# Kernel tuning notes

Hardware: AMD Instinct MI355X
Metric: run time of the kernel (lower is better)

## Reference

```python
import jax, jax.numpy as jnp
import numpy as np

B, T, H, O, L = 64, 512, 256, 128, 2


def setup_inputs() -> dict:
    key = jax.random.key(0)
    ks = jax.random.split(key, 12)
    s = lambda k, shape, scale=0.05: jax.random.normal(k, shape, dtype=jnp.float32) * scale
    return {
        "encoder_outputs": jax.random.normal(ks[0], (B, T, H), dtype=jnp.float32),
        "h0": jax.random.normal(ks[1], (L, B, H), dtype=jnp.float32),
        "c0": jax.random.normal(ks[2], (L, B, H), dtype=jnp.float32),
        "actions": jax.random.randint(ks[3], (B, T), 0, O, dtype=jnp.int32),
        "embedding": jax.random.uniform(ks[4], (O, H), dtype=jnp.float32, minval=-1.0, maxval=1.0),
        "Wih": s(ks[5], (L, 4 * H, H)),
        "Whh": s(ks[6], (L, 4 * H, H)),
        "bih": jnp.zeros((L, 4 * H), jnp.float32),
        "bhh": jnp.zeros((L, 4 * H), jnp.float32),
        "W_attn": s(ks[7], (H, H)),
        "b_attn": jnp.zeros((H,), jnp.float32),
        "W_concat": s(ks[8], (H, 2 * H)),
        "b_concat": jnp.zeros((H,), jnp.float32),
        "W_out": s(ks[9], (O, H)),
        "W_critic": s(ks[10], (O, O)),
        "b_critic": jnp.zeros((O,), jnp.float32),
    }


def _run_lstm(x, h0, c0, Wih, Whh, bih, bhh):
    # x: [B, T, H]; stacked-layer LSTM, PyTorch gate order (i, f, g, o)
    xs = jnp.swapaxes(x, 0, 1)  # [T, B, H]
    for l in range(Wih.shape[0]):
        Wi_l, Wh_l = Wih[l].T, Whh[l].T
        b_l = bih[l] + bhh[l]
        def step(carry, xt, Wi=Wi_l, Wh=Wh_l, b=b_l):
            h, c = carry
            g = xt @ Wi + h @ Wh + b
            i, f, gg, o = jnp.split(g, 4, axis=-1)
            c = jax.nn.sigmoid(f) * c + jax.nn.sigmoid(i) * jnp.tanh(gg)
            h = jax.nn.sigmoid(o) * jnp.tanh(c)
            return (h, c), h
        _, xs = jax.lax.scan(step, (h0[l], c0[l]), xs)
    return jnp.swapaxes(xs, 0, 1)  # [B, T, H]


def reference(encoder_outputs, h0, c0, actions, embedding, Wih, Whh, bih, bhh,
              W_attn, b_attn, W_concat, b_concat, W_out, W_critic, b_critic):
    # Teacher forcing: input at step t is action[t-1], step 0 input is token 0.
    ids = jnp.concatenate([jnp.zeros((actions.shape[0], 1), actions.dtype), actions[:, :-1]], axis=1)
    emb = embedding[ids]  # [B, T, H]
    out = _run_lstm(emb, h0, c0, Wih, Whh, bih, bhh)  # [B, T, H]

    # Luong attention, batched over all decode steps (same math as per-step bmm)
    keys = encoder_outputs @ W_attn.T + b_attn  # [B, S, H]
    scores = jnp.einsum("bth,bsh->bts", out, keys)
    weights = jax.nn.softmax(scores, axis=-1)
    ctx = jnp.einsum("bts,bsh->bth", weights, encoder_outputs)
    out = jnp.tanh(jnp.concatenate([out, ctx], axis=-1) @ W_concat.T + b_concat)

    logits = out @ W_out.T  # [B, T, O]
    qvalues = logits @ W_critic.T + b_critic  # [B, T, O]
    values = jnp.sum(qvalues * logits, axis=-1)  # [B, T]
    decoder_action = actions.astype(jnp.float32)
    return decoder_action, logits, values
```

## Files before the change

kernel.cpp:

```cpp
#include <hip/hip_runtime.h>
#include <stdint.h>

#define BB   64
#define TT   512
#define HT   256
#define OO   128
#define GATES 1024

#define PREG 10
#define PLDS 4
#define PSTR 2
#define UREG (2*PREG)
#define ULDS (2*PLDS)
#define AGDEPTH 16

typedef _Float16 half_t;
typedef _Float16 half2_t __attribute__((ext_vector_type(2)));
typedef float    f32x4  __attribute__((ext_vector_type(4)));
typedef unsigned long long u64;

__device__ __forceinline__ half2_t h2_(unsigned int x) {
    return __builtin_bit_cast(half2_t, x);
}
#define WG_BARRIER() do { __builtin_amdgcn_s_waitcnt(0xC07F); \
                          __builtin_amdgcn_s_barrier(); } while (0)

__device__ __forceinline__ float fast_sig(float x) {
    return __builtin_amdgcn_rcpf(1.0f + __expf(-x));
}
__device__ __forceinline__ float fast_tanh(float x) {
    float t = __expf(2.0f * x);
    return 1.0f - 2.0f * __builtin_amdgcn_rcpf(t + 1.0f);
}

__device__ __forceinline__ unsigned int scload(const unsigned int* p) {
    unsigned long long a = (unsigned long long)p;
    unsigned int w;
    asm volatile("global_load_dword %0, %1, off sc0 sc1\n\ts_waitcnt vmcnt(0)"
                 : "=v"(w) : "v"(a) : "memory");
    return w;
}
__device__ __forceinline__ u64 scload64(const u64* p) {
    unsigned long long a = (unsigned long long)p;
    u64 w;
    asm volatile("global_load_dwordx2 %0, %1, off sc0 sc1\n\ts_waitcnt vmcnt(0)"
                 : "=v"(w) : "v"(a) : "memory");
    return w;
}
__device__ __forceinline__ void scload64x4(
    const u64* p0, const u64* p1, const u64* p2, const u64* p3,
    u64& w0, u64& w1, u64& w2, u64& w3)
{
    unsigned long long a0 = (unsigned long long)p0;
    unsigned long long a1 = (unsigned long long)p1;
    unsigned long long a2 = (unsigned long long)p2;
    unsigned long long a3 = (unsigned long long)p3;
    asm volatile(
        "global_load_dwordx2 %0, %4, off sc0 sc1\n\t"
        "global_load_dwordx2 %1, %5, off sc0 sc1\n\t"
        "global_load_dwordx2 %2, %6, off sc0 sc1\n\t"
        "global_load_dwordx2 %3, %7, off sc0 sc1\n\t"
        "s_waitcnt vmcnt(0)"
        : "=v"(w0), "=v"(w1), "=v"(w2), "=v"(w3)
        : "v"(a0), "v"(a1), "v"(a2), "v"(a3) : "memory");
}

#define PAIR_DOT(wa0, wb0, wa1, wb1, h4)                                  \
    do {                                                                   \
        a0 = __builtin_amdgcn_fdot2(h2_((wa0).x), h2_((h4).x), a0, false); \
        a0 = __builtin_amdgcn_fdot2(h2_((wa0).y), h2_((h4).y), a0, false); \
        a1 = __builtin_amdgcn_fdot2(h2_((wa0).z), h2_((h4).x), a1, false); \
        a1 = __builtin_amdgcn_fdot2(h2_((wa0).w), h2_((h4).y), a1, false); \
        a2 = __builtin_amdgcn_fdot2(h2_((wb0).x), h2_((h4).x), a2, false); \
        a2 = __builtin_amdgcn_fdot2(h2_((wb0).y), h2_((h4).y), a2, false); \
        a3 = __builtin_amdgcn_fdot2(h2_((wb0).z), h2_((h4).x), a3, false); \
        a3 = __builtin_amdgcn_fdot2(h2_((wb0).w), h2_((h4).y), a3, false); \
        a0 = __builtin_amdgcn_fdot2(h2_((wa1).x), h2_((h4).z), a0, false); \
        a0 = __builtin_amdgcn_fdot2(h2_((wa1).y), h2_((h4).w), a0, false); \
        a1 = __builtin_amdgcn_fdot2(h2_((wa1).z), h2_((h4).z), a1, false); \
        a1 = __builtin_amdgcn_fdot2(h2_((wa1).w), h2_((h4).w), a1, false); \
        a2 = __builtin_amdgcn_fdot2(h2_((wb1).x), h2_((h4).z), a2, false); \
        a2 = __builtin_amdgcn_fdot2(h2_((wb1).y), h2_((h4).w), a2, false); \
        a3 = __builtin_amdgcn_fdot2(h2_((wb1).z), h2_((h4).z), a3, false); \
        a3 = __builtin_amdgcn_fdot2(h2_((wb1).w), h2_((h4).w), a3, false); \
    } while (0)

#define DOT_PHASE()                                                        \
    do {                                                                   \
        _Pragma("unroll 2")                                                \
        for (int p = 0; p < PSTR; p++) {                                   \
            uint4 wa0 = Ws[(p * 4 + 0) * 512 + tid];                       \
            uint4 wb0 = Ws[(p * 4 + 1) * 512 + tid];                       \
            uint4 wa1 = Ws[(p * 4 + 2) * 512 + tid];                       \
            uint4 wb1 = Ws[(p * 4 + 3) * 512 + tid];                       \
            uint4 h4  = hp4[hb + PREG + PLDS + p];                         \
            PAIR_DOT(wa0, wb0, wa1, wb1, h4);                              \
        }                                                                  \
        _Pragma("unroll")                                                  \
        for (int p = 0; p < PLDS; p++) {                                   \
            uint4 wa0 = Wlh[(p * 4 + 0) * 512 + tid];                      \
            uint4 wb0 = Wlh[(p * 4 + 1) * 512 + tid];                      \
            uint4 wa1 = Wlh[(p * 4 + 2) * 512 + tid];                      \
            uint4 wb1 = Wlh[(p * 4 + 3) * 512 + tid];                      \
            uint4 h4  = hp4[hb + PREG + p];                                \
            PAIR_DOT(wa0, wb0, wa1, wb1, h4);                              \
        }                                                                  \
        _Pragma("unroll")                                                  \
        for (int p = 0; p < PREG; p++) {                                   \
            uint4 h4 = hp4[hb + p];                                        \
            PAIR_DOT(wreg[4 * p], wreg[4 * p + 1],                         \
                     wreg[4 * p + 2], wreg[4 * p + 3], h4);                \
        }                                                                  \
    } while (0)

__global__ __launch_bounds__(256) void embed_kernel(
    const int* __restrict__ actions, const float* __restrict__ emb_table,
    float* __restrict__ X, float* __restrict__ dact)
{
    int row = blockIdx.x;
    int t = row & (TT - 1);
    int id = (t == 0) ? 0 : actions[row - 1];
    X[(int64_t)row * HT + threadIdx.x] = emb_table[(int64_t)id * HT + threadIdx.x];
    if (threadIdx.x == 0) dact[row] = (float)actions[row];
}

__global__ __launch_bounds__(256) void repack_w_kernel(
    const float* __restrict__ Whh, const float* __restrict__ Wih,
    uint4* __restrict__ Wpkh)
{
    int idx = blockIdx.x * 256 + threadIdx.x;
    int g   = idx & 32767;
    int l   = idx >> 15;
    int tid = g & 511;
    int ab  = (g >> 9) & 1;
    int u   = (g >> 10) & 31;
    int s = tid >> 8, q = tid & 255;
    int r0 = 4 * q + 2 * ab;
    int k  = 128 * s + 4 * u;
    const float* base = (l == 0) ? Whh
                      : (l == 1) ? Whh + (int64_t)GATES * HT
                                 : Wih + (int64_t)GATES * HT;
    const float4 a = *(const float4*)(base + (int64_t)r0 * HT + k);
    const float4 b = *(const float4*)(base + (int64_t)(r0 + 1) * HT + k);
    half2_t p0 = {(half_t)a.x, (half_t)a.y};
    half2_t p1 = {(half_t)a.z, (half_t)a.w};
    half2_t p2 = {(half_t)b.x, (half_t)b.y};
    half2_t p3 = {(half_t)b.z, (half_t)b.w};
    uint4 o;
    o.x = __builtin_bit_cast(unsigned int, p0);
    o.y = __builtin_bit_cast(unsigned int, p1);
    o.z = __builtin_bit_cast(unsigned int, p2);
    o.w = __builtin_bit_cast(unsigned int, p3);
    Wpkh[idx] = o;
}

__global__ __launch_bounds__(256) void hxzero_kernel(
    uint4* __restrict__ HX4, u64* __restrict__ AGU,
    unsigned int* __restrict__ CCTR)
{
    int i = blockIdx.x * 256 + threadIdx.x;
    HX4[i] = make_uint4(0u, 0u, 0u, 0u);
    if (i < AGDEPTH * 64 * 1024) AGU[i] = 0ull;
    if (i < 64) CCTR[i] = 0u;
}

template<bool TRANS_B, int ACT>
__global__ __launch_bounds__(256) void mfma_gemm_kernel(
    const float* __restrict__ A, const float* __restrict__ Bm,
    float* __restrict__ C,
    int K, int lda, int ldb, int ldc,
    int64_t sA, int64_t sB, int64_t sC,
    const float* __restrict__ bias1, const float* __restrict__ bias2)
{
    constexpr int BM = 128, BN = 128, BK = 32;
    constexpr int LDT = BK + 8;
    __shared__ __align__(16) half_t Asl[BM * LDT];
    __shared__ __align__(16) half_t Bsl[BN * LDT];

    const int tid  = threadIdx.x;
    const int wave = tid >> 6;
    const int lane = tid & 63;
    const int wm = (wave & 1) * 64;
    const int wn = (wave >> 1) * 64;
    const int m0 = blockIdx.y * BM;
    const int n0 = blockIdx.x * BN;
    A  += (int64_t)blockIdx.z * sA;
    Bm += (int64_t)blockIdx.z * sB;
    C  += (int64_t)blockIdx.z * sC;

    const int fm = lane & 15;
    const int qd = lane >> 4;

    f32x4 acc[4][4] = {};

    for (int k0 = 0; k0 < K; k0 += BK) {
        #pragma unroll
        for (int i = 0; i < 4; i++) {
            int idx = tid + i * 256;
            int r  = idx >> 3;
            int kq = idx & 7;
            float4 v = *(const float4*)(A + (int64_t)(m0 + r) * lda + k0 + kq * 4);
            half_t* d = &Asl[r * LDT + kq * 4];
            d[0] = (half_t)v.x; d[1] = (half_t)v.y;
            d[2] = (half_t)v.z; d[3] = (half_t)v.w;
        }
        if (TRANS_B) {
            #pragma unroll
            for (int i = 0; i < 4; i++) {
                int idx = tid + i * 256;
                int r  = idx >> 3;
                int kq = idx & 7;
                float4 v = *(const float4*)(Bm + (int64_t)(n0 + r) * ldb + k0 + kq * 4);
                half_t* d = &Bsl[r * LDT + kq * 4];
                d[0] = (half_t)v.x; d[1] = (half_t)v.y;
                d[2] = (half_t)v.z; d[3] = (half_t)v.w;
            }
        } else {
            #pragma unroll
            for (int i = 0; i < 4; i++) {
                int idx = tid + i * 256;
                int kk = idx >> 5;
                int nq = idx & 31;
                float4 v = *(const float4*)(Bm + (int64_t)(k0 + kk) * ldb + n0 + nq * 4);
                Bsl[(nq * 4 + 0) * LDT + kk] = (half_t)v.x;
                Bsl[(nq * 4 + 1) * LDT + kk] = (half_t)v.y;
                Bsl[(nq * 4 + 2) * LDT + kk] = (half_t)v.z;
                Bsl[(nq * 4 + 3) * LDT + kk] = (half_t)v.w;
            }
        }
        __syncthreads();

        typedef _Float16 f16x8 __attribute__((ext_vector_type(8)));
        f16x8 af[4], bf[4];
        #pragma unroll
        for (int t = 0; t < 4; t++)
            af[t] = *(const f16x8*)&Asl[(wm + t * 16 + fm) * LDT + qd * 8];
        #pragma unroll
        for (int t = 0; t < 4; t++)
            bf[t] = *(const f16x8*)&Bsl[(wn + t * 16 + fm) * LDT + qd * 8];
        #pragma unroll
        for (int mt = 0; mt < 4; mt++)
            #pragma unroll
            for (int nt = 0; nt < 4; nt++)
                acc[mt][nt] = __builtin_amdgcn_mfma_f32_16x16x32_f16(
                                  af[mt], bf[nt], acc[mt][nt], 0, 0, 0);
        __syncthreads();
    }

    #pragma unroll
    for (int nt = 0; nt < 4; nt++) {
        int n = n0 + wn + nt * 16 + fm;
        float bv = 0.0f;
        if (bias1) bv += bias1[n];
        if (bias2) bv += bias2[n];
        #pragma unroll
        for (int mt = 0; mt < 4; mt++) {
            #pragma unroll
            for (int r = 0; r < 4; r++) {
                int m = m0 + wm + mt * 16 + qd * 4 + r;
                float v = acc[mt][nt][r] + bv;
                if (ACT == 1) v = tanhf(v);
                C[(int64_t)m * ldc + n] = v;
            }
        }
    }
}

template<bool TRANS_B, int ACT>
__global__ __launch_bounds__(256) void gemm128_kernel(
    const float* __restrict__ A, const float* __restrict__ Bm,
    float* __restrict__ C,
    int K, int lda, int ldb, int ldc,
    int64_t sA, int64_t sB, int64_t sC,
    const float* __restrict__ bias1, const float* __restrict__ bias2)
{
    constexpr int BM = 128, BN = 128, BK = 16;
    __shared__ __align__(16) float As[BK][BM + 4];
    __shared__ __align__(16) float Bs[BK][BN + 4];

    const int tid = threadIdx.x;
    const int m0 = blockIdx.y * BM;
    const int n0 = blockIdx.x * BN;
    A  += (int64_t)blockIdx.z * sA;
    Bm += (int64_t)blockIdx.z * sB;
    C  += (int64_t)blockIdx.z * sC;

    const int tm = tid & 15;
    const int tn = tid >> 4;

    float acc[8][8] = {};

    for (int k0 = 0; k0 < K; k0 += BK) {
        #pragma unroll
        for (int i = 0; i < 2; i++) {
            int idx = tid + i * 256;
            int ar = idx >> 2;
            int ak = (idx & 3) * 4;
            const float4 v = *(const float4*)(A + (int64_t)(m0 + ar) * lda + k0 + ak);
            As[ak + 0][ar] = v.x; As[ak + 1][ar] = v.y;
            As[ak + 2][ar] = v.z; As[ak + 3][ar] = v.w;
        }
        if (TRANS_B) {
            #pragma unroll
            for (int i = 0; i < 2; i++) {
                int idx = tid + i * 256;
                int br = idx >> 2;
                int bk = (idx & 3) * 4;
                const float4 v = *(const float4*)(Bm + (int64_t)(n0 + br) * ldb + k0 + bk);
                Bs[bk + 0][br] = v.x; Bs[bk + 1][br] = v.y;
                Bs[bk + 2][br] = v.z; Bs[bk + 3][br] = v.w;
            }
        } else {
            #pragma unroll
            for (int i = 0; i < 2; i++) {
                int idx = tid + i * 256;
                int bk = idx >> 5;
                int bn = (idx & 31) * 4;
                const float4 v = *(const float4*)(Bm + (int64_t)(k0 + bk) * ldb + n0 + bn);
                *(float4*)&Bs[bk][bn] = v;
            }
        }
        __syncthreads();

        #pragma unroll
        for (int k = 0; k < BK; k++) {
            float a[8], b[8];
            *(float4*)&a[0] = *(const float4*)&As[k][tm * 8];
            *(float4*)&a[4] = *(const float4*)&As[k][tm * 8 + 4];
            *(float4*)&b[0] = *(const float4*)&Bs[k][tn * 8];
            *(float4*)&b[4] = *(const float4*)&Bs[k][tn * 8 + 4];
            #pragma unroll
            for (int i = 0; i < 8; i++)
                #pragma unroll
                for (int j = 0; j < 8; j++)
                    acc[i][j] += a[i] * b[j];
        }
        __syncthreads();
    }

    float bv[8];
    #pragma unroll
    for (int j = 0; j < 8; j++) {
        int n = n0 + tn * 8 + j;
        float b = 0.0f;
        if (bias1) b += bias1[n];
        if (bias2) b += bias2[n];
        bv[j] = b;
    }
    #pragma unroll
    for (int i = 0; i < 8; i++) {
        int64_t m = m0 + tm * 8 + i;
        float o[8];
        #pragma unroll
        for (int j = 0; j < 8; j++) {
            float v = acc[i][j] + bv[j];
            if (ACT == 1) v = tanhf(v);
            o[j] = v;
        }
        *(float4*)(C + m * ldc + n0 + tn * 8)     = make_float4(o[0], o[1], o[2], o[3]);
        *(float4*)(C + m * ldc + n0 + tn * 8 + 4) = make_float4(o[4], o[5], o[6], o[7]);
    }
}

__global__ __launch_bounds__(512)
__attribute__((amdgpu_waves_per_eu(2, 2)))
void fused_rec_kernel(
    const float* __restrict__ Ag0,
    const uint4* __restrict__ Wpk,
    const float* __restrict__ h0l,
    const float* __restrict__ c0l,
    const float* __restrict__ bih,
    const float* __restrict__ bhh,
    float* __restrict__ cat,
    unsigned int* __restrict__ HX,
    u64* __restrict__ AGU,
    unsigned int* __restrict__ CCTR)
{
    const int bid  = blockIdx.x;
    const int role = bid >> 6;
    const int b    = bid & 63;
    const int tid  = threadIdx.x;
    const int s    = tid >> 8;
    const int q    = tid & 255;

    __shared__ __align__(16) uint4          Wlh[ULDS * 2 * 512];
    __shared__ __align__(16) float          gsh2[2 * GATES];
    __shared__ __align__(16) float          agsh[2][GATES];
    __shared__ __align__(16) unsigned short hsh[HT];

    const uint4* Wb = Wpk + (role == 0 ? 0 : (role == 1 ? 2 : 1)) * 32768;

    uint4 wreg[2 * UREG];
    #pragma unroll
    for (int u = 0; u < UREG; u++) {
        wreg[2 * u]     = Wb[(u * 2 + 0) * 512 + tid];
        wreg[2 * u + 1] = Wb[(u * 2 + 1) * 512 + tid];
    }
    #pragma unroll
    for (int v = 0; v < ULDS; v++) {
        Wlh[(v * 2 + 0) * 512 + tid] = Wb[((UREG + v) * 2 + 0) * 512 + tid];
        Wlh[(v * 2 + 1) * 512 + tid] = Wb[((UREG + v) * 2 + 1) * 512 + tid];
    }
    const uint4* __restrict__ Ws = Wb + (UREG + ULDS) * 2 * 512;
    const uint4* hp4 = (const uint4*)hsh;
    const int hb = 16 * s;

    if (role == 0) {
        if (tid < HT) {
            half_t hv = (half_t)h0l[b * HT + tid];
            hsh[tid] = __builtin_bit_cast(unsigned short, hv);
        }
        float c = (tid < HT) ? c0l[b * HT + tid] : 0.0f;
        const float* AgB = Ag0 + (int64_t)b * TT * GATES;
        unsigned int* HXb = HX + (int64_t)b * TT * HT;
        __syncthreads();

        #pragma unroll 1
        for (int st = 0; st < TT; st++) {
            float4 aval = make_float4(0.f, 0.f, 0.f, 0.f);
            if (s == 0) aval = *(const float4*)(AgB + (int64_t)st * GATES + 4 * q);
            float a0 = 0.f, a1 = 0.f, a2 = 0.f, a3 = 0.f;
            DOT_PHASE();
            a0 += aval.x; a1 += aval.y; a2 += aval.z; a3 += aval.w;
            *(float4*)&gsh2[s * GATES + 4 * q] = make_float4(a0, a1, a2, a3);
            WG_BARRIER();
            if (tid < HT) {
                float gi = gsh2[tid]          + gsh2[GATES + tid];
                float gf = gsh2[HT + tid]     + gsh2[GATES + HT + tid];
                float gg = gsh2[2 * HT + tid] + gsh2[GATES + 2 * HT + tid];
                float go = gsh2[3 * HT + tid] + gsh2[GATES + 3 * HT + tid];
                c = fast_sig(gf) * c + fast_sig(gi) * fast_tanh(gg);
                float h = fast_sig(go) * fast_tanh(c);
                half_t hh = (half_t)h;
                unsigned short hb16 = __builtin_bit_cast(unsigned short, hh);
                hsh[tid] = hb16;
                atomicExch(HXb + (int64_t)st * HT + tid,
                           ((unsigned)(st + 1) << 16) | (unsigned)hb16);
            }
            WG_BARRIER();
        }
    } else if (role == 1) {
        float bi_ = 0.f, bf_ = 0.f, bg_ = 0.f, bo_ = 0.f;
        if (tid < HT) {
            bi_ = bih[GATES + tid]          + bhh[GATES + tid];
            bf_ = bih[GATES + HT + tid]     + bhh[GATES + HT + tid];
            bg_ = bih[GATES + 2 * HT + tid] + bhh[GATES + 2 * HT + tid];
            bo_ = bih[GATES + 3 * HT + tid] + bhh[GATES + 3 * HT + tid];
        }
        const unsigned int* HXb = HX + (int64_t)b * TT * HT;
        __syncthreads();

        #pragma unroll 1
        for (int st = 0; st < TT; st++) {
            if ((st & 3) == 0 && st >= AGDEPTH && tid == 0) {
                while (scload(&CCTR[b]) < (unsigned)(st - (AGDEPTH - 4))) {}
            }
            if (tid < HT) {
                const unsigned int* src = HXb + (int64_t)st * HT + tid;
                unsigned int w = scload(src);
                while ((w >> 16) != (unsigned)(st + 1)) w = scload(src);
                hsh[tid] = (unsigned short)(w & 0xffffu);
            }
            WG_BARRIER();
            float a0 = 0.f, a1 = 0.f, a2 = 0.f, a3 = 0.f;
            DOT_PHASE();
            *(float4*)&gsh2[s * GATES + 4 * q] = make_float4(a0, a1, a2, a3);
            WG_BARRIER();
            if (tid < HT) {
                u64 hi = ((u64)(st + 1)) << 32;
                u64* dst = AGU + (int64_t)((st & (AGDEPTH - 1)) * 64 + b) * 1024;
                float v0 = gsh2[tid]          + gsh2[GATES + tid]          + bi_;
                float v1 = gsh2[HT + tid]     + gsh2[GATES + HT + tid]     + bf_;
                float v2 = gsh2[2 * HT + tid] + gsh2[GATES + 2 * HT + tid] + bg_;
                float v3 = gsh2[3 * HT + tid] + gsh2[GATES + 3 * HT + tid] + bo_;
                atomicExch(&dst[tid],          hi | (u64)__float_as_uint(v0));
                atomicExch(&dst[HT + tid],     hi | (u64)__float_as_uint(v1));
                atomicExch(&dst[2 * HT + tid], hi | (u64)__float_as_uint(v2));
                atomicExch(&dst[3 * HT + tid], hi | (u64)__float_as_uint(v3));
            }
        }
    } else {
        if (tid < HT) {
            half_t hv = (half_t)h0l[BB * HT + b * HT + tid];
            hsh[tid] = __builtin_bit_cast(unsigned short, hv);
        }
        float c = (tid < HT) ? c0l[BB * HT + b * HT + tid] : 0.0f;
        __syncthreads();
        if (tid >= 256) {
            int i = tid - 256;
            const u64* src = AGU + (int64_t)b * 1024;
            u64 w0, w1, w2, w3;
            scload64x4(src + i, src + i + 256, src + i + 512, src + i + 768,
                       w0, w1, w2, w3);
            while ((unsigned)(w0 >> 32) != 1u) w0 = scload64(src + i);
            while ((unsigned)(w1 >> 32) != 1u) w1 = scload64(src + i + 256);
            while ((unsigned)(w2 >> 32) != 1u) w2 = scload64(src + i + 512);
            while ((unsigned)(w3 >> 32) != 1u) w3 = scload64(src + i + 768);
            agsh[0][i]       = __uint_as_float((unsigned)w0);
            agsh[0][i + 256] = __uint_as_float((unsigned)w1);
            agsh[0][i + 512] = __uint_as_float((unsigned)w2);
            agsh[0][i + 768] = __uint_as_float((unsigned)w3);
        }
        WG_BARRIER();

        #pragma unroll 1
        for (int st = 0; st < TT; st++) {
            float a0 = 0.f, a1 = 0.f, a2 = 0.f, a3 = 0.f;
            DOT_PHASE();
            *(float4*)&gsh2[s * GATES + 4 * q] = make_float4(a0, a1, a2, a3);
            WG_BARRIER();
            if (tid < HT) {
                const float* ag = agsh[st & 1];
                float gi = gsh2[tid]          + gsh2[GATES + tid]          + ag[tid];
                float gf = gsh2[HT + tid]     + gsh2[GATES + HT + tid]     + ag[HT + tid];
                float gg = gsh2[2 * HT + tid] + gsh2[GATES + 2 * HT + tid] + ag[2 * HT + tid];
                float go = gsh2[3 * HT + tid] + gsh2[GATES + 3 * HT + tid] + ag[3 * HT + tid];
                c = fast_sig(gf) * c + fast_sig(gi) * fast_tanh(gg);
                float h = fast_sig(go) * fast_tanh(c);
                hsh[tid] = __builtin_bit_cast(unsigned short, (half_t)h);
                cat[((int64_t)b * TT + st) * (2 * HT) + tid] = h;
            } else {
                if ((st & 3) == 3 && tid == 256)
                    atomicExch(&CCTR[b], (unsigned)(st + 1));
                if (st + 1 < TT) {
                    int i = tid - 256;
                    int sl = (st + 1) & (AGDEPTH - 1);
                    unsigned expect = (unsigned)(st + 2);
                    const u64* src = AGU + (int64_t)(sl * 64 + b) * 1024;
                    u64 w0, w1, w2, w3;
                    scload64x4(src + i, src + i + 256, src + i + 512, src + i + 768,
                               w0, w1, w2, w3);
                    while ((unsigned)(w0 >> 32) != expect) w0 = scload64(src + i);
                    while ((unsigned)(w1 >> 32) != expect) w1 = scload64(src + i + 256);
                    while ((unsigned)(w2 >> 32) != expect) w2 = scload64(src + i + 512);
                    while ((unsigned)(w3 >> 32) != expect) w3 = scload64(src + i + 768);
                    float* d = agsh[(st + 1) & 1];
                    d[i]       = __uint_as_float((unsigned)w0);
                    d[i + 256] = __uint_as_float((unsigned)w1);
                    d[i + 512] = __uint_as_float((unsigned)w2);
                    d[i + 768] = __uint_as_float((unsigned)w3);
                }
            }
            WG_BARRIER();
        }
    }
}

__global__ __launch_bounds__(256) void softmax512_kernel(float* __restrict__ S)
{
    int row = blockIdx.x * 4 + (threadIdx.x >> 6);
    int lane = threadIdx.x & 63;
    float* p = S + (int64_t)row * 512 + lane * 8;
    float4 v0 = *(float4*)p;
    float4 v1 = *(float4*)(p + 4);
    float m = fmaxf(fmaxf(fmaxf(v0.x, v0.y), fmaxf(v0.z, v0.w)),
                    fmaxf(fmaxf(v1.x, v1.y), fmaxf(v1.z, v1.w)));
    #pragma unroll
    for (int off = 32; off; off >>= 1) m = fmaxf(m, __shfl_xor(m, off));
    v0.x = __expf(v0.x - m); v0.y = __expf(v0.y - m);
    v0.z = __expf(v0.z - m); v0.w = __expf(v0.w - m);
    v1.x = __expf(v1.x - m); v1.y = __expf(v1.y - m);
    v1.z = __expf(v1.z - m); v1.w = __expf(v1.w - m);
    float s = v0.x + v0.y + v0.z + v0.w + v1.x + v1.y + v1.z + v1.w;
    #pragma unroll
    for (int off = 32; off; off >>= 1) s += __shfl_xor(s, off);
    float inv = 1.0f / s;
    v0.x *= inv; v0.y *= inv; v0.z *= inv; v0.w *= inv;
    v1.x *= inv; v1.y *= inv; v1.z *= inv; v1.w *= inv;
    *(float4*)p = v0;
    *(float4*)(p + 4) = v1;
}

__global__ __launch_bounds__(256) void values_kernel(
    const float* __restrict__ Q, const float* __restrict__ L, float* __restrict__ V)
{
    int row = blockIdx.x * 4 + (threadIdx.x >> 6);
    int lane = threadIdx.x & 63;
    float2 q = *(const float2*)(Q + (int64_t)row * OO + lane * 2);
    float2 l = *(const float2*)(L + (int64_t)row * OO + lane * 2);
    float s = q.x * l.x + q.y * l.y;
    #pragma unroll
    for (int off = 32; off; off >>= 1) s += __shfl_xor(s, off);
    if (lane == 0) V[row] = s;
}

extern "C" void kernel_launch(void* const* d_in, const int* in_sizes, int n_in,
                              void* d_out, int out_size, void* d_ws, size_t ws_size,
                              hipStream_t stream)
{
    const float* enc      = (const float*)d_in[0];
    const float* h0       = (const float*)d_in[1];
    const float* c0       = (const float*)d_in[2];
    const int*   actions  = (const int*)  d_in[3];
    const float* emb_t    = (const float*)d_in[4];
    const float* Wih      = (const float*)d_in[5];
    const float* Whh      = (const float*)d_in[6];
    const float* bih      = (const float*)d_in[7];
    const float* bhh      = (const float*)d_in[8];
    const float* W_attn   = (const float*)d_in[9];
    const float* b_attn   = (const float*)d_in[10];
    const float* W_concat = (const float*)d_in[11];
    const float* b_concat = (const float*)d_in[12];
    const float* W_out    = (const float*)d_in[13];
    const float* W_critic = (const float*)d_in[14];
    const float* b_critic = (const float*)d_in[15];
    (void)in_sizes; (void)n_in; (void)out_size; (void)ws_size;

    const int M = BB * TT;

    float* out    = (float*)d_out;
    float* dact   = out;
    float* logits = out + M;
    float* values = out + M + (int64_t)M * OO;

    float* ws    = (float*)d_ws;
    float* gates = ws;
    float* xbuf  = ws + 33554432;
    float* cat   = ws + 41943040;
    float* keysR = ws + 58720256;
    float* keys  = keysR;
    uint4* Wpkh  = (uint4*)keysR;
    u64*   AGU   = (u64*)(ws + 59500000);
    unsigned int* CCTR = (unsigned int*)(ws + 61600000);
    unsigned int* HX   = (unsigned int*)xbuf;
    float* scores = gates;
    float* qv     = gates;
    float* dec    = xbuf;

    hipLaunchKernelGGL(embed_kernel, dim3(M), dim3(256), 0, stream,
                       actions, emb_t, xbuf, dact);
    hipLaunchKernelGGL(repack_w_kernel, dim3(384), dim3(256), 0, stream,
                       Whh, Wih, Wpkh);
    hipLaunchKernelGGL((mfma_gemm_kernel<true, 0>), dim3(8, 256, 1), dim3(256), 0, stream,
                       xbuf, Wih, gates, HT, HT, HT, GATES,
                       (int64_t)0, (int64_t)0, (int64_t)0, bih, bhh);
    hipLaunchKernelGGL(hxzero_kernel, dim3(8192), dim3(256), 0, stream,
                       (uint4*)HX, AGU, CCTR);
    hipLaunchKernelGGL(fused_rec_kernel, dim3(192), dim3(512), 0, stream,
                       gates, Wpkh, h0, c0, bih, bhh, cat, HX, AGU, CCTR);
    hipLaunchKernelGGL((mfma_gemm_kernel<true, 0>), dim3(2, 256, 1), dim3(256), 0, stream,
                       enc, W_attn, keys, HT, HT, HT, HT,
                       (int64_t)0, (int64_t)0, (int64_t)0, b_attn, (const float*)nullptr);
    hipLaunchKernelGGL((mfma_gemm_kernel<true, 0>), dim3(4, 4, BB), dim3(256), 0, stream,
                       cat, keys, scores, HT, 2 * HT, HT, TT,
                       (int64_t)TT * 2 * HT, (int64_t)TT * HT, (int64_t)TT * TT,
                       (const float*)nullptr, (const float*)nullptr);
    hipLaunchKernelGGL(softmax512_kernel, dim3(M / 4), dim3(256), 0, stream, scores);
    hipLaunchKernelGGL((mfma_gemm_kernel<false, 0>), dim3(2, 4, BB), dim3(256), 0, stream,
                       scores, enc, cat + HT, TT, TT, HT, 2 * HT,
                       (int64_t)TT * TT, (int64_t)TT * HT, (int64_t)TT * 2 * HT,
                       (const float*)nullptr, (const float*)nullptr);
    hipLaunchKernelGGL((mfma_gemm_kernel<true, 1>), dim3(2, 256, 1), dim3(256), 0, stream,
                       cat, W_concat, dec, 2 * HT, 2 * HT, 2 * HT, HT,
                       (int64_t)0, (int64_t)0, (int64_t)0, b_concat, (const float*)nullptr);
    hipLaunchKernelGGL((gemm128_kernel<true, 0>), dim3(1, 256, 1), dim3(256), 0, stream,
                       dec, W_out, logits, HT, HT, HT, OO,
                       (int64_t)0, (int64_t)0, (int64_t)0,
                       (const float*)nullptr, (const float*)nullptr);
    hipLaunchKernelGGL((gemm128_kernel<true, 0>), dim3(1, 256, 1), dim3(256), 0, stream,
                       logits, W_critic, qv, OO, OO, OO, OO,
                       (int64_t)0, (int64_t)0, (int64_t)0, b_critic, (const float*)nullptr);
    hipLaunchKernelGGL(values_kernel, dim3(M / 4), dim3(256), 0, stream,
                       qv, logits, values);
}
```

Before: 1.615 ms.

## Split layer-1 input projection role across two blocks per batch and prefetch gates

The role that computes the layer-1 input projection (Wih[1] times layer-0 h) is now split across two workgroups per batch row, each handling 512 gate rows with a new weight packing. This halves per-block work on that stage of the wavefront pipeline, and the grid grows from 192 to 256 blocks. The layer-1 recurrence block also issues its polling loads for the next step's precomputed gates before its dot phase and waits on them afterwards, hiding global latency behind compute. The cost is more blocks that must stay co-resident for the spin-wait protocol, plus more atomic traffic.

```diff
diff --git a/kernel.cpp b/kernel.cpp
--- a/kernel.cpp
+++ b/kernel.cpp
@@ -63,6 +63,30 @@
         "s_waitcnt vmcnt(0)"
         : "=v"(w0), "=v"(w1), "=v"(w2), "=v"(w3)
         : "v"(a0), "v"(a1), "v"(a2), "v"(a3) : "memory");
+}
+__device__ __forceinline__ void scload64x4_issue(
+    const u64* p0, const u64* p1, const u64* p2, const u64* p3,
+    u64& w0, u64& w1, u64& w2, u64& w3)
+{
+    unsigned long long a0 = (unsigned long long)p0;
+    unsigned long long a1 = (unsigned long long)p1;
+    unsigned long long a2 = (unsigned long long)p2;
+    unsigned long long a3 = (unsigned long long)p3;
+    asm volatile(
+        "global_load_dwordx2 %0, %4, off sc0 sc1\n\t"
+        "global_load_dwordx2 %1, %5, off sc0 sc1\n\t"
+        "global_load_dwordx2 %2, %6, off sc0 sc1\n\t"
+        "global_load_dwordx2 %3, %7, off sc0 sc1"
+        : "=v"(w0), "=v"(w1), "=v"(w2), "=v"(w3)
+        : "v"(a0), "v"(a1), "v"(a2), "v"(a3) : "memory");
+}
+
+__device__ __forceinline__ float dot8(float acc, uint4 wv, uint4 h4) {
+    acc = __builtin_amdgcn_fdot2(h2_(wv.x), h2_(h4.x), acc, false);
+    acc = __builtin_amdgcn_fdot2(h2_(wv.y), h2_(h4.y), acc, false);
+    acc = __builtin_amdgcn_fdot2(h2_(wv.z), h2_(h4.z), acc, false);
+    acc = __builtin_amdgcn_fdot2(h2_(wv.w), h2_(h4.w), acc, false);
+    return acc;
 }
 
 #define PAIR_DOT(wa0, wb0, wa1, wb1, h4)                                  \
@@ -131,27 +155,51 @@
     int idx = blockIdx.x * 256 + threadIdx.x;
     int g   = idx & 32767;
     int l   = idx >> 15;
-    int tid = g & 511;
-    int ab  = (g >> 9) & 1;
-    int u   = (g >> 10) & 31;
-    int s = tid >> 8, q = tid & 255;
-    int r0 = 4 * q + 2 * ab;
-    int k  = 128 * s + 4 * u;
-    const float* base = (l == 0) ? Whh
-                      : (l == 1) ? Whh + (int64_t)GATES * HT
-                                 : Wih + (int64_t)GATES * HT;
-    const float4 a = *(const float4*)(base + (int64_t)r0 * HT + k);
-    const float4 b = *(const float4*)(base + (int64_t)(r0 + 1) * HT + k);
-    half2_t p0 = {(half_t)a.x, (half_t)a.y};
-    half2_t p1 = {(half_t)a.z, (half_t)a.w};
-    half2_t p2 = {(half_t)b.x, (half_t)b.y};
-    half2_t p3 = {(half_t)b.z, (half_t)b.w};
-    uint4 o;
-    o.x = __builtin_bit_cast(unsigned int, p0);
-    o.y = __builtin_bit_cast(unsigned int, p1);
-    o.z = __builtin_bit_cast(unsigned int, p2);
-    o.w = __builtin_bit_cast(unsigned int, p3);
-    Wpkh[idx] = o;
+    const float* base;
+    int row, k;
+    if (l < 2) {
+        int tid = g & 511;
+        int ab  = (g >> 9) & 1;
+        int u   = (g >> 10) & 31;
+        int s = tid >> 8, q = tid & 255;
+        row = 4 * q + 2 * ab;
+        k   = 128 * s + 4 * u;
+        base = Whh + (int64_t)l * (GATES * HT);
+        const float4 a = *(const float4*)(base + (int64_t)row * HT + k);
+        const float4 b = *(const float4*)(base + (int64_t)(row + 1) * HT + k);
+        half2_t p0 = {(half_t)a.x, (half_t)a.y};
+        half2_t p1 = {(half_t)a.z, (half_t)a.w};
+        half2_t p2 = {(half_t)b.x, (half_t)b.y};
+        half2_t p3 = {(half_t)b.z, (half_t)b.w};
+        uint4 o;
+        o.x = __builtin_bit_cast(unsigned int, p0);
+        o.y = __builtin_bit_cast(unsigned int, p1);
+        o.z = __builtin_bit_cast(unsigned int, p2);
+        o.w = __builtin_bit_cast(unsigned int, p3);
+        Wpkh[idx] = o;
+        return;
+    }
+    {
+        int t = g & 511;
+        int m = (g >> 9) & 31;
+        int h = g >> 14;
+        int s = t >> 8, q = t & 255;
+        row = 512 * h + 2 * q + (m >= 16 ? 1 : 0);
+        k   = 128 * s + 8 * (m & 15);
+        base = Wih + (int64_t)GATES * HT;
+        const float4 a = *(const float4*)(base + (int64_t)row * HT + k);
+        const float4 b = *(const float4*)(base + (int64_t)row * HT + k + 4);
+        half2_t p0 = {(half_t)a.x, (half_t)a.y};
+        half2_t p1 = {(half_t)a.z, (half_t)a.w};
+        half2_t p2 = {(half_t)b.x, (half_t)b.y};
+        half2_t p3 = {(half_t)b.z, (half_t)b.w};
+        uint4 o;
+        o.x = __builtin_bit_cast(unsigned int, p0);
+        o.y = __builtin_bit_cast(unsigned int, p1);
+        o.z = __builtin_bit_cast(unsigned int, p2);
+        o.w = __builtin_bit_cast(unsigned int, p3);
+        Wpkh[idx] = o;
+    }
 }
 
 __global__ __launch_bounds__(256) void hxzero_kernel(
@@ -376,36 +424,38 @@
     u64* __restrict__ AGU,
     unsigned int* __restrict__ CCTR)
 {
-    const int bid  = blockIdx.x;
-    const int role = bid >> 6;
-    const int b    = bid & 63;
-    const int tid  = threadIdx.x;
-    const int s    = tid >> 8;
-    const int q    = tid & 255;
+    const int bid = blockIdx.x;
+    int role, b, half = 0;
+    if (bid < 64)       { role = 0; b = bid; }
+    else if (bid < 192) { role = 1; b = (bid - 64) & 63; half = (bid - 64) >> 6; }
+    else                { role = 2; b = bid - 192; }
+    const int tid = threadIdx.x;
+    const int s   = tid >> 8;
+    const int q   = tid & 255;
 
     __shared__ __align__(16) uint4          Wlh[ULDS * 2 * 512];
     __shared__ __align__(16) float          gsh2[2 * GATES];
     __shared__ __align__(16) float          agsh[2][GATES];
     __shared__ __align__(16) unsigned short hsh[HT];
 
-    const uint4* Wb = Wpk + (role == 0 ? 0 : (role == 1 ? 2 : 1)) * 32768;
-
-    uint4 wreg[2 * UREG];
-    #pragma unroll
-    for (int u = 0; u < UREG; u++) {
-        wreg[2 * u]     = Wb[(u * 2 + 0) * 512 + tid];
-        wreg[2 * u + 1] = Wb[(u * 2 + 1) * 512 + tid];
-    }
-    #pragma unroll
-    for (int v = 0; v < ULDS; v++) {
-        Wlh[(v * 2 + 0) * 512 + tid] = Wb[((UREG + v) * 2 + 0) * 512 + tid];
-        Wlh[(v * 2 + 1) * 512 + tid] = Wb[((UREG + v) * 2 + 1) * 512 + tid];
-    }
-    const uint4* __restrict__ Ws = Wb + (UREG + ULDS) * 2 * 512;
     const uint4* hp4 = (const uint4*)hsh;
     const int hb = 16 * s;
 
     if (role == 0) {
+        const uint4* Wb = Wpk;
+        uint4 wreg[2 * UREG];
+        #pragma unroll
+        for (int u = 0; u < UREG; u++) {
+            wreg[2 * u]     = Wb[(u * 2 + 0) * 512 + tid];
+            wreg[2 * u + 1] = Wb[(u * 2 + 1) * 512 + tid];
+        }
+        #pragma unroll
+        for (int v = 0; v < ULDS; v++) {
+            Wlh[(v * 2 + 0) * 512 + tid] = Wb[((UREG + v) * 2 + 0) * 512 + tid];
+            Wlh[(v * 2 + 1) * 512 + tid] = Wb[((UREG + v) * 2 + 1) * 512 + tid];
+        }
+        const uint4* __restrict__ Ws = Wb + (UREG + ULDS) * 2 * 512;
+
         if (tid < HT) {
             half_t hv = (half_t)h0l[b * HT + tid];
             hsh[tid] = __builtin_bit_cast(unsigned short, hv);
@@ -440,14 +490,16 @@
             WG_BARRIER();
         }
     } else if (role == 1) {
-        float bi_ = 0.f, bf_ = 0.f, bg_ = 0.f, bo_ = 0.f;
-        if (tid < HT) {
-            bi_ = bih[GATES + tid]          + bhh[GATES + tid];
-            bf_ = bih[GATES + HT + tid]     + bhh[GATES + HT + tid];
-            bg_ = bih[GATES + 2 * HT + tid] + bhh[GATES + 2 * HT + tid];
-            bo_ = bih[GATES + 3 * HT + tid] + bhh[GATES + 3 * HT + tid];
-        }
+        const uint4* WbB = Wpk + 2 * 32768 + (half * 32) * 512 + tid;
+        uint4 wr[16];
+        #pragma unroll
+        for (int m = 0; m < 16; m++) wr[m] = WbB[m * 512];
+        #pragma unroll
+        for (int m = 0; m < 16; m++) Wlh[m * 512 + tid] = WbB[(16 + m) * 512];
+
+        float brow = bih[GATES + 512 * half + tid] + bhh[GATES + 512 * half + tid];
         const unsigned int* HXb = HX + (int64_t)b * TT * HT;
+        const uint4* wlB = Wlh + tid;
         __syncthreads();
 
         #pragma unroll 1
@@ -462,24 +514,38 @@
                 hsh[tid] = (unsigned short)(w & 0xffffu);
             }
             WG_BARRIER();
-            float a0 = 0.f, a1 = 0.f, a2 = 0.f, a3 = 0.f;
-            DOT_PHASE();
-            *(float4*)&gsh2[s * GATES + 4 * q] = make_float4(a0, a1, a2, a3);
+            float a0 = 0.f, a1 = 0.f;
+            #pragma unroll
+            for (int u = 0; u < 16; u++) {
+                uint4 h4 = hp4[16 * s + u];
+                a0 = dot8(a0, wr[u], h4);
+                a1 = dot8(a1, wlB[u * 512], h4);
+            }
+            gsh2[s * 512 + 2 * q]     = a0;
+            gsh2[s * 512 + 2 * q + 1] = a1;
             WG_BARRIER();
-            if (tid < HT) {
-                u64 hi = ((u64)(st + 1)) << 32;
-                u64* dst = AGU + (int64_t)((st & (AGDEPTH - 1)) * 64 + b) * 1024;
-                float v0 = gsh2[tid]          + gsh2[GATES + tid]          + bi_;
-                float v1 = gsh2[HT + tid]     + gsh2[GATES + HT + tid]     + bf_;
-                float v2 = gsh2[2 * HT + tid] + gsh2[GATES + 2 * HT + tid] + bg_;
-                float v3 = gsh2[3 * HT + tid] + gsh2[GATES + 3 * HT + tid] + bo_;
-                atomicExch(&dst[tid],          hi | (u64)__float_as_uint(v0));
-                atomicExch(&dst[HT + tid],     hi | (u64)__float_as_uint(v1));
-                atomicExch(&dst[2 * HT + tid], hi | (u64)__float_as_uint(v2));
-                atomicExch(&dst[3 * HT + tid], hi | (u64)__float_as_uint(v3));
+            {
+                float v = gsh2[tid] + gsh2[512 + tid] + brow;
+                u64 w = (((u64)(st + 1)) << 32) | (u64)__float_as_uint(v);
+                atomicExch(AGU + (int64_t)((st & (AGDEPTH - 1)) * 64 + b) * 1024
+                               + 512 * half + tid, w);
             }
         }
     } else {
+        const uint4* Wb = Wpk + 32768;
+        uint4 wreg[2 * UREG];
+        #pragma unroll
+        for (int u = 0; u < UREG; u++) {
+            wreg[2 * u]     = Wb[(u * 2 + 0) * 512 + tid];
+            wreg[2 * u + 1] = Wb[(u * 2 + 1) * 512 + tid];
+        }
+        #pragma unroll
+        for (int v = 0; v < ULDS; v++) {
+            Wlh[(v * 2 + 0) * 512 + tid] = Wb[((UREG + v) * 2 + 0) * 512 + tid];
+            Wlh[(v * 2 + 1) * 512 + tid] = Wb[((UREG + v) * 2 + 1) * 512 + tid];
+        }
+        const uint4* __restrict__ Ws = Wb + (UREG + ULDS) * 2 * 512;
+
         if (tid < HT) {
             half_t hv = (half_t)h0l[BB * HT + b * HT + tid];
             hsh[tid] = __builtin_bit_cast(unsigned short, hv);
@@ -505,9 +571,17 @@
 
         #pragma unroll 1
         for (int st = 0; st < TT; st++) {
+            u64 pw0 = 0, pw1 = 0, pw2 = 0, pw3 = 0;
+            if (tid >= 256 && st + 1 < TT) {
+                int i = tid - 256;
+                int sl = (st + 1) & (AGDEPTH - 1);
+                const u64* src = AGU + (int64_t)(sl * 64 + b) * 1024;
+                scload64x4_issue(src + i, src + i + 256, src + i + 512,
+                                 src + i + 768, pw0, pw1, pw2, pw3);
+            }
             float a0 = 0.f, a1 = 0.f, a2 = 0.f, a3 = 0.f;
             DOT_PHASE();
-            *(float4*)&gsh2[s * GATES + 4 * q] = make_float4(a0, a1, a2, a3);
+            *(f32x4*)&gsh2[s * GATES + 4 * q] = f32x4{a0, a1, a2, a3};
             WG_BARRIER();
             if (tid < HT) {
                 const float* ag = agsh[st & 1];
@@ -527,18 +601,16 @@
                     int sl = (st + 1) & (AGDEPTH - 1);
                     unsigned expect = (unsigned)(st + 2);
                     const u64* src = AGU + (int64_t)(sl * 64 + b) * 1024;
-                    u64 w0, w1, w2, w3;
-                    scload64x4(src + i, src + i + 256, src + i + 512, src + i + 768,
-                               w0, w1, w2, w3);
-                    while ((unsigned)(w0 >> 32) != expect) w0 = scload64(src + i);
-                    while ((unsigned)(w1 >> 32) != expect) w1 = scload64(src + i + 256);
-                    while ((unsigned)(w2 >> 32) != expect) w2 = scload64(src + i + 512);
-                    while ((unsigned)(w3 >> 32) != expect) w3 = scload64(src + i + 768);
+                    asm volatile("s_waitcnt vmcnt(0)" ::: "memory");
+                    while ((unsigned)(pw0 >> 32) != expect) pw0 = scload64(src + i);
+                    while ((unsigned)(pw1 >> 32) != expect) pw1 = scload64(src + i + 256);
+                    while ((unsigned)(pw2 >> 32) != expect) pw2 = scload64(src + i + 512);
+                    while ((unsigned)(pw3 >> 32) != expect) pw3 = scload64(src + i + 768);
                     float* d = agsh[(st + 1) & 1];
-                    d[i]       = __uint_as_float((unsigned)w0);
-                    d[i + 256] = __uint_as_float((unsigned)w1);
-                    d[i + 512] = __uint_as_float((unsigned)w2);
-                    d[i + 768] = __uint_as_float((unsigned)w3);
+                    d[i]       = __uint_as_float((unsigned)pw0);
+                    d[i + 256] = __uint_as_float((unsigned)pw1);
+                    d[i + 512] = __uint_as_float((unsigned)pw2);
+                    d[i + 768] = __uint_as_float((unsigned)pw3);
                 }
             }
             WG_BARRIER();
@@ -636,7 +708,7 @@
                        (int64_t)0, (int64_t)0, (int64_t)0, bih, bhh);
     hipLaunchKernelGGL(hxzero_kernel, dim3(8192), dim3(256), 0, stream,
                        (uint4*)HX, AGU, CCTR);
-    hipLaunchKernelGGL(fused_rec_kernel, dim3(192), dim3(512), 0, stream,
+    hipLaunchKernelGGL(fused_rec_kernel, dim3(256), dim3(512), 0, stream,
                        gates, Wpkh, h0, c0, bih, bhh, cat, HX, AGU, CCTR);
     hipLaunchKernelGGL((mfma_gemm_kernel<true, 0>), dim3(2, 256, 1), dim3(256), 0, stream,
                        enc, W_attn, keys, HT, HT, HT, HT,
```

Measured after the change: 1.656 ms. +2.5%, slower.

## Prefetch next-step gate inputs before dot phase and add sleep backoff to spins

Applied to the files above, without the earlier changes.

The layer-1 consumer now issues the loads for the next step's precomputed input-gate values before the dot-product phase and waits on them only afterwards, so the global-memory latency overlaps with compute. Spin-wait loops gain s_sleep backoff to cut memory polling pressure. The layer-0 producer's gate publishing moves to the upper half of threads, and the dot-phase order is changed to start with register-resident weights. The risks are that sleep adds wake-up latency on the critical recurrent path, and that the prefetch relies on inline asm with no waitcnt, which depends on correct vmcnt handling.

```diff
diff --git a/kernel.cpp b/kernel.cpp
--- a/kernel.cpp
+++ b/kernel.cpp
@@ -61,6 +61,22 @@
         "global_load_dwordx2 %2, %6, off sc0 sc1\n\t"
         "global_load_dwordx2 %3, %7, off sc0 sc1\n\t"
         "s_waitcnt vmcnt(0)"
+        : "=v"(w0), "=v"(w1), "=v"(w2), "=v"(w3)
+        : "v"(a0), "v"(a1), "v"(a2), "v"(a3) : "memory");
+}
+__device__ __forceinline__ void scload64x4_issue(
+    const u64* p0, const u64* p1, const u64* p2, const u64* p3,
+    u64& w0, u64& w1, u64& w2, u64& w3)
+{
+    unsigned long long a0 = (unsigned long long)p0;
+    unsigned long long a1 = (unsigned long long)p1;
+    unsigned long long a2 = (unsigned long long)p2;
+    unsigned long long a3 = (unsigned long long)p3;
+    asm volatile(
+        "global_load_dwordx2 %0, %4, off sc0 sc1\n\t"
+        "global_load_dwordx2 %1, %5, off sc0 sc1\n\t"
+        "global_load_dwordx2 %2, %6, off sc0 sc1\n\t"
+        "global_load_dwordx2 %3, %7, off sc0 sc1"
         : "=v"(w0), "=v"(w1), "=v"(w2), "=v"(w3)
         : "v"(a0), "v"(a1), "v"(a2), "v"(a3) : "memory");
 }
@@ -87,14 +103,11 @@
 
 #define DOT_PHASE()                                                        \
     do {                                                                   \
-        _Pragma("unroll 2")                                                \
-        for (int p = 0; p < PSTR; p++) {                                   \
-            uint4 wa0 = Ws[(p * 4 + 0) * 512 + tid];                       \
-            uint4 wb0 = Ws[(p * 4 + 1) * 512 + tid];                       \
-            uint4 wa1 = Ws[(p * 4 + 2) * 512 + tid];                       \
-            uint4 wb1 = Ws[(p * 4 + 3) * 512 + tid];                       \
-            uint4 h4  = hp4[hb + PREG + PLDS + p];                         \
-            PAIR_DOT(wa0, wb0, wa1, wb1, h4);                              \
+        _Pragma("unroll")                                                  \
+        for (int p = 0; p < PREG; p++) {                                   \
+            uint4 h4 = hp4[hb + p];                                        \
+            PAIR_DOT(wreg[4 * p], wreg[4 * p + 1],                         \
+                     wreg[4 * p + 2], wreg[4 * p + 3], h4);                \
         }                                                                  \
         _Pragma("unroll")                                                  \
         for (int p = 0; p < PLDS; p++) {                                   \
@@ -105,11 +118,14 @@
             uint4 h4  = hp4[hb + PREG + p];                                \
             PAIR_DOT(wa0, wb0, wa1, wb1, h4);                              \
         }                                                                  \
-        _Pragma("unroll")                                                  \
-        for (int p = 0; p < PREG; p++) {                                   \
-            uint4 h4 = hp4[hb + p];                                        \
-            PAIR_DOT(wreg[4 * p], wreg[4 * p + 1],                         \
-                     wreg[4 * p + 2], wreg[4 * p + 3], h4);                \
+        _Pragma("unroll 2")                                                \
+        for (int p = 0; p < PSTR; p++) {                                   \
+            uint4 wa0 = Ws[(p * 4 + 0) * 512 + tid];                       \
+            uint4 wb0 = Ws[(p * 4 + 1) * 512 + tid];                       \
+            uint4 wa1 = Ws[(p * 4 + 2) * 512 + tid];                       \
+            uint4 wb1 = Ws[(p * 4 + 3) * 512 + tid];                       \
+            uint4 h4  = hp4[hb + PREG + PLDS + p];                         \
+            PAIR_DOT(wa0, wb0, wa1, wb1, h4);                              \
         }                                                                  \
     } while (0)
 
@@ -441,11 +457,12 @@
         }
     } else if (role == 1) {
         float bi_ = 0.f, bf_ = 0.f, bg_ = 0.f, bo_ = 0.f;
-        if (tid < HT) {
-            bi_ = bih[GATES + tid]          + bhh[GATES + tid];
-            bf_ = bih[GATES + HT + tid]     + bhh[GATES + HT + tid];
-            bg_ = bih[GATES + 2 * HT + tid] + bhh[GATES + 2 * HT + tid];
-            bo_ = bih[GATES + 3 * HT + tid] + bhh[GATES + 3 * HT + tid];
+        if (tid >= 256) {
+            int i = tid - 256;
+            bi_ = bih[GATES + i]          + bhh[GATES + i];
+            bf_ = bih[GATES + HT + i]     + bhh[GATES + HT + i];
+            bg_ = bih[GATES + 2 * HT + i] + bhh[GATES + 2 * HT + i];
+            bo_ = bih[GATES + 3 * HT + i] + bhh[GATES + 3 * HT + i];
         }
         const unsigned int* HXb = HX + (int64_t)b * TT * HT;
         __syncthreads();
@@ -453,12 +470,19 @@
         #pragma unroll 1
         for (int st = 0; st < TT; st++) {
             if ((st & 3) == 0 && st >= AGDEPTH && tid == 0) {
-                while (scload(&CCTR[b]) < (unsigned)(st - (AGDEPTH - 4))) {}
+                unsigned cc = scload(&CCTR[b]);
+                while (cc < (unsigned)(st - (AGDEPTH - 4))) {
+                    __builtin_amdgcn_s_sleep(2);
+                    cc = scload(&CCTR[b]);
+                }
             }
             if (tid < HT) {
                 const unsigned int* src = HXb + (int64_t)st * HT + tid;
                 unsigned int w = scload(src);
-                while ((w >> 16) != (unsigned)(st + 1)) w = scload(src);
+                while ((w >> 16) != (unsigned)(st + 1)) {
+                    __builtin_amdgcn_s_sleep(1);
+                    w = scload(src);
+                }
                 hsh[tid] = (unsigned short)(w & 0xffffu);
             }
             WG_BARRIER();
@@ -466,17 +490,18 @@
             DOT_PHASE();
             *(float4*)&gsh2[s * GATES + 4 * q] = make_float4(a0, a1, a2, a3);
             WG_BARRIER();
-            if (tid < HT) {
+            if (tid >= 256) {
+                int i = tid - 256;
                 u64 hi = ((u64)(st + 1)) << 32;
                 u64* dst = AGU + (int64_t)((st & (AGDEPTH - 1)) * 64 + b) * 1024;
-                float v0 = gsh2[tid]          + gsh2[GATES + tid]          + bi_;
-                float v1 = gsh2[HT + tid]     + gsh2[GATES + HT + tid]     + bf_;
-                float v2 = gsh2[2 * HT + tid] + gsh2[GATES + 2 * HT + tid] + bg_;
-                float v3 = gsh2[3 * HT + tid] + gsh2[GATES + 3 * HT + tid] + bo_;
-                atomicExch(&dst[tid],          hi | (u64)__float_as_uint(v0));
-                atomicExch(&dst[HT + tid],     hi | (u64)__float_as_uint(v1));
-                atomicExch(&dst[2 * HT + tid], hi | (u64)__float_as_uint(v2));
-                atomicExch(&dst[3 * HT + tid], hi | (u64)__float_as_uint(v3));
+                float v0 = gsh2[i]          + gsh2[GATES + i]          + bi_;
+                float v1 = gsh2[HT + i]     + gsh2[GATES + HT + i]     + bf_;
+                float v2 = gsh2[2 * HT + i] + gsh2[GATES + 2 * HT + i] + bg_;
+                float v3 = gsh2[3 * HT + i] + gsh2[GATES + 3 * HT + i] + bo_;
+                atomicExch(&dst[i],          hi | (u64)__float_as_uint(v0));
+                atomicExch(&dst[HT + i],     hi | (u64)__float_as_uint(v1));
+                atomicExch(&dst[2 * HT + i], hi | (u64)__float_as_uint(v2));
+                atomicExch(&dst[3 * HT + i], hi | (u64)__float_as_uint(v3));
             }
         }
     } else {
@@ -492,10 +517,10 @@
             u64 w0, w1, w2, w3;
             scload64x4(src + i, src + i + 256, src + i + 512, src + i + 768,
                        w0, w1, w2, w3);
-            while ((unsigned)(w0 >> 32) != 1u) w0 = scload64(src + i);
-            while ((unsigned)(w1 >> 32) != 1u) w1 = scload64(src + i + 256);
-            while ((unsigned)(w2 >> 32) != 1u) w2 = scload64(src + i + 512);
-            while ((unsigned)(w3 >> 32) != 1u) w3 = scload64(src + i + 768);
+            while ((unsigned)(w0 >> 32) != 1u) { __builtin_amdgcn_s_sleep(1); w0 = scload64(src + i); }
+            while ((unsigned)(w1 >> 32) != 1u) { __builtin_amdgcn_s_sleep(1); w1 = scload64(src + i + 256); }
+            while ((unsigned)(w2 >> 32) != 1u) { __builtin_amdgcn_s_sleep(1); w2 = scload64(src + i + 512); }
+            while ((unsigned)(w3 >> 32) != 1u) { __builtin_amdgcn_s_sleep(1); w3 = scload64(src + i + 768); }
             agsh[0][i]       = __uint_as_float((unsigned)w0);
             agsh[0][i + 256] = __uint_as_float((unsigned)w1);
             agsh[0][i + 512] = __uint_as_float((unsigned)w2);
@@ -505,9 +530,17 @@
 
         #pragma unroll 1
         for (int st = 0; st < TT; st++) {
+            u64 pw0 = 0, pw1 = 0, pw2 = 0, pw3 = 0;
+            if (tid >= 256 && st + 1 < TT) {
+                int i = tid - 256;
+                int sl = (st + 1) & (AGDEPTH - 1);
+                const u64* src = AGU + (int64_t)(sl * 64 + b) * 1024;
+                scload64x4_issue(src + i, src + i + 256, src + i + 512,
+                                 src + i + 768, pw0, pw1, pw2, pw3);
+            }
             float a0 = 0.f, a1 = 0.f, a2 = 0.f, a3 = 0.f;
             DOT_PHASE();
-            *(float4*)&gsh2[s * GATES + 4 * q] = make_float4(a0, a1, a2, a3);
+            *(f32x4*)&gsh2[s * GATES + 4 * q] = f32x4{a0, a1, a2, a3};
             WG_BARRIER();
             if (tid < HT) {
                 const float* ag = agsh[st & 1];
@@ -527,18 +560,16 @@
                     int sl = (st + 1) & (AGDEPTH - 1);
                     unsigned expect = (unsigned)(st + 2);
                     const u64* src = AGU + (int64_t)(sl * 64 + b) * 1024;
-                    u64 w0, w1, w2, w3;
-                    scload64x4(src + i, src + i + 256, src + i + 512, src + i + 768,
-                               w0, w1, w2, w3);
-                    while ((unsigned)(w0 >> 32) != expect) w0 = scload64(src + i);
-                    while ((unsigned)(w1 >> 32) != expect) w1 = scload64(src + i + 256);
-                    while ((unsigned)(w2 >> 32) != expect) w2 = scload64(src + i + 512);
-                    while ((unsigned)(w3 >> 32) != expect) w3 = scload64(src + i + 768);
+                    asm volatile("s_waitcnt vmcnt(0)" ::: "memory");
+                    while ((unsigned)(pw0 >> 32) != expect) { __builtin_amdgcn_s_sleep(1); pw0 = scload64(src + i); }
+                    while ((unsigned)(pw1 >> 32) != expect) { __builtin_amdgcn_s_sleep(1); pw1 = scload64(src + i + 256); }
+                    while ((unsigned)(pw2 >> 32) != expect) { __builtin_amdgcn_s_sleep(1); pw2 = scload64(src + i + 512); }
+                    while ((unsigned)(pw3 >> 32) != expect) { __builtin_amdgcn_s_sleep(1); pw3 = scload64(src + i + 768); }
                     float* d = agsh[(st + 1) & 1];
-                    d[i]       = __uint_as_float((unsigned)w0);
-                    d[i + 256] = __uint_as_float((unsigned)w1);
-                    d[i + 512] = __uint_as_float((unsigned)w2);
-                    d[i + 768] = __uint_as_float((unsigned)w3);
+                    d[i]       = __uint_as_float((unsigned)pw0);
+                    d[i + 256] = __uint_as_float((unsigned)pw1);
+                    d[i + 512] = __uint_as_float((unsigned)pw2);
+                    d[i + 768] = __uint_as_float((unsigned)pw3);
                 }
             }
             WG_BARRIER();
```

Result: faster. 1.550 ms (-4.0%).
